# Kernel optimization log

Measured on AMD Instinct MI355X. Metric: run time of the kernel, lower is better.

## Reference

```python
import jax, jax.numpy as jnp
import numpy as np

NUM_SYM = 50000
NUM_HERB = 50000
N_NODES = NUM_SYM + NUM_HERB
DIM = 128
N_EDGES = 3200000
N_LAYERS = 2


def setup_inputs() -> dict:
    key = jax.random.key(0)
    k1, k2, k3, k4, k5 = jax.random.split(key, 5)
    sym_emb = jax.random.normal(k1, (NUM_SYM, DIM), dtype=jnp.float32)
    herb_emb = jax.random.normal(k2, (NUM_HERB, DIM), dtype=jnp.float32)
    adj_rows = jax.random.randint(k3, (N_EDGES,), 0, N_NODES, dtype=jnp.int32)
    adj_cols = jax.random.randint(k4, (N_EDGES,), 0, N_NODES, dtype=jnp.int32)
    # normalized-Laplacian values are positive; uniform stands in for D^-1/2 A D^-1/2 entries
    adj_vals = jax.random.uniform(k5, (N_EDGES,), dtype=jnp.float32)
    return {"sym_emb": sym_emb, "herb_emb": herb_emb,
            "adj_rows": adj_rows, "adj_cols": adj_cols, "adj_vals": adj_vals}


def _spmm(rows, cols, vals, x):
    # sparse [N,N] @ dense [N,D]: gather source rows, scale, scatter-add to dest rows
    msgs = vals[:, None] * x[cols]              # [E, D]
    return jax.ops.segment_sum(msgs, rows, num_segments=N_NODES)


def reference(sym_emb, herb_emb, adj_rows, adj_cols, adj_vals):
    ego = jnp.concatenate([sym_emb, herb_emb], axis=0)   # [N, D]
    acc = ego
    e = ego
    for _ in range(N_LAYERS):
        e = _spmm(adj_rows, adj_cols, adj_vals, e)
        acc = acc + e
    all_emb = acc / jnp.float32(N_LAYERS + 1)            # mean over stacked layers
    return all_emb[:NUM_SYM], all_emb[NUM_SYM:]
```

## Files before the change

### kernel.cpp

```cpp
#include <hip/hip_runtime.h>

#define NUM_SYM 50000
#define NUM_HERB 50000
#define N_NODES (NUM_SYM + NUM_HERB)
#define DIM 128
#define NB_BUCKETS ((N_NODES + 255) / 256)
#define CHUNK 8192
#define PAD 16

typedef float floatx4 __attribute__((ext_vector_type(4)));

__device__ __forceinline__ float bf2f(unsigned short u) {
    return __uint_as_float((unsigned)u << 16);
}
__device__ __forceinline__ unsigned short f2bf(float f) {
    unsigned u = __float_as_uint(f);
    unsigned r = (u + 0x7FFFu + ((u >> 16) & 1u)) >> 16;
    return (unsigned short)r;
}

__global__ __launch_bounds__(256) void to_bf16(
    const float* __restrict__ sym, const float* __restrict__ herb,
    ushort* __restrict__ xbf)
{
    int i = blockIdx.x * 256 + threadIdx.x;
    const int n4 = N_NODES * DIM / 4;
    if (i >= n4) return;
    const int sym4 = NUM_SYM * DIM / 4;
    float4 v = (i < sym4) ? reinterpret_cast<const float4*>(sym)[i]
                          : reinterpret_cast<const float4*>(herb)[i - sym4];
    ushort4 o;
    o.x = f2bf(v.x); o.y = f2bf(v.y); o.z = f2bf(v.z); o.w = f2bf(v.w);
    reinterpret_cast<ushort4*>(xbf)[i] = o;
}


__global__ __launch_bounds__(1024) void hist_buckets(
    const int* __restrict__ rows, int E, int* __restrict__ bucket_cnt)
{
    __shared__ int h[NB_BUCKETS];
    for (int i = threadIdx.x; i < NB_BUCKETS; i += 1024) h[i] = 0;
    __syncthreads();
    int start = blockIdx.x * CHUNK;
    int end   = min(start + CHUNK, E);
    for (int e = start + threadIdx.x; e < end; e += 1024)
        atomicAdd(&h[rows[e] >> 8], 1);
    __syncthreads();
    for (int i = threadIdx.x; i < NB_BUCKETS; i += 1024)
        if (h[i]) atomicAdd(&bucket_cnt[i * PAD], h[i]);
}

__global__ __launch_bounds__(512) void scan_buckets(
    const int* __restrict__ cnt, int* __restrict__ off, int* __restrict__ cursor)
{
    __shared__ int s[512];
    int t = threadIdx.x;
    int v = (t < NB_BUCKETS) ? cnt[t * PAD] : 0;
    s[t] = v;
    __syncthreads();
    for (int o = 1; o < 512; o <<= 1) {
        int x = (t >= o) ? s[t - o] : 0;
        __syncthreads();
        s[t] += x;
        __syncthreads();
    }
    if (t < NB_BUCKETS) { off[t] = s[t] - v; cursor[t * PAD] = s[t] - v; }
    if (t == NB_BUCKETS - 1) off[NB_BUCKETS] = s[t];
}

__global__ __launch_bounds__(1024) void scatter_buckets(
    const int* __restrict__ rows, const int* __restrict__ cols,
    const float* __restrict__ vals, int E,
    int* __restrict__ cursor, int2* __restrict__ bucketed)
{
    __shared__ int lh[NB_BUCKETS];
    __shared__ int lbase[NB_BUCKETS];
    for (int i = threadIdx.x; i < NB_BUCKETS; i += 1024) lh[i] = 0;
    __syncthreads();
    int start = blockIdx.x * CHUNK;
    int end   = min(start + CHUNK, E);
    for (int e = start + threadIdx.x; e < end; e += 1024)
        atomicAdd(&lh[rows[e] >> 8], 1);
    __syncthreads();
    for (int i = threadIdx.x; i < NB_BUCKETS; i += 1024) {
        int c = lh[i];
        lbase[i] = c ? atomicAdd(&cursor[i * PAD], c) : 0;
        lh[i] = 0;
    }
    __syncthreads();
    for (int e = start + threadIdx.x; e < end; e += 1024) {
        int r = rows[e];
        int key = r >> 8;
        int pos = lbase[key] + atomicAdd(&lh[key], 1);
        bucketed[pos] = make_int2(((r & 255) << 17) | cols[e],
                                  __float_as_int(vals[e]));
    }
}

__global__ __launch_bounds__(1024) void bucket_to_csr(
    const int2* __restrict__ bucketed, const int* __restrict__ off,
    int* __restrict__ csr, int* __restrict__ rowptr)
{
    __shared__ int h[256];
    int b = blockIdx.x, t = threadIdx.x;
    int s0 = off[b], s1 = off[b + 1];
    if (t < 256) h[t] = 0;
    __syncthreads();
    for (int j = s0 + t; j < s1; j += 1024)
        atomicAdd(&h[(unsigned)bucketed[j].x >> 17], 1);
    __syncthreads();
    int v = (t < 256) ? h[t] : 0;
    for (int o = 1; o < 256; o <<= 1) {
        int x = (t < 256 && t >= o) ? h[t - o] : 0;
        __syncthreads();
        if (t < 256) h[t] += x;
        __syncthreads();
    }
    if (t < 256) {
        int r = b * 256 + t;
        if (r < N_NODES) rowptr[r] = s0 + (h[t] - v);
    }
    __syncthreads();
    if (t < 256) h[t] -= v;
    __syncthreads();
    for (int j = s0 + t; j < s1; j += 1024) {
        int2 rec = bucketed[j];
        int key = (unsigned)rec.x >> 17;
        int pos = s0 + atomicAdd(&h[key], 1);
        unsigned vb = (unsigned)f2bf(__int_as_float(rec.y));
        csr[pos] = (int)((vb << 17) | ((unsigned)rec.x & 0x1FFFFu));
    }
}

__device__ __forceinline__ float unpack_val(int p) {
    return __uint_as_float(((unsigned)p >> 17) << 16);
}

template <bool FUSE_MEAN>
__global__ __launch_bounds__(256) void spmm_csr_bf16(
    const int* __restrict__ csr, const int* __restrict__ rowptr, int E,
    const ushort* __restrict__ xbf,
    const float* __restrict__ sym, const float* __restrict__ herb,
    const ushort* __restrict__ e1bf,
    void* __restrict__ outp)
{
    int wave = blockIdx.x * 4 + (threadIdx.x >> 6);
    int half = (threadIdx.x >> 5) & 1;
    int lane = threadIdx.x & 31;
    int r = wave * 2 + half;
    if (r >= N_NODES) return;

    int j   = rowptr[r];
    int end = (r + 1 < N_NODES) ? rowptr[r + 1] : E;

    float4 acc = make_float4(0.f, 0.f, 0.f, 0.f);
    for (; j + 7 < end; j += 8) {
        int p0 = __builtin_nontemporal_load(csr + j);
        int p1 = __builtin_nontemporal_load(csr + j + 1);
        int p2 = __builtin_nontemporal_load(csr + j + 2);
        int p3 = __builtin_nontemporal_load(csr + j + 3);
        int p4 = __builtin_nontemporal_load(csr + j + 4);
        int p5 = __builtin_nontemporal_load(csr + j + 5);
        int p6 = __builtin_nontemporal_load(csr + j + 6);
        int p7 = __builtin_nontemporal_load(csr + j + 7);
        ushort4 m0 = reinterpret_cast<const ushort4*>(xbf + (size_t)(p0 & 0x1FFFF) * DIM)[lane];
        ushort4 m1 = reinterpret_cast<const ushort4*>(xbf + (size_t)(p1 & 0x1FFFF) * DIM)[lane];
        ushort4 m2 = reinterpret_cast<const ushort4*>(xbf + (size_t)(p2 & 0x1FFFF) * DIM)[lane];
        ushort4 m3 = reinterpret_cast<const ushort4*>(xbf + (size_t)(p3 & 0x1FFFF) * DIM)[lane];
        ushort4 m4 = reinterpret_cast<const ushort4*>(xbf + (size_t)(p4 & 0x1FFFF) * DIM)[lane];
        ushort4 m5 = reinterpret_cast<const ushort4*>(xbf + (size_t)(p5 & 0x1FFFF) * DIM)[lane];
        ushort4 m6 = reinterpret_cast<const ushort4*>(xbf + (size_t)(p6 & 0x1FFFF) * DIM)[lane];
        ushort4 m7 = reinterpret_cast<const ushort4*>(xbf + (size_t)(p7 & 0x1FFFF) * DIM)[lane];
        float v0 = unpack_val(p0), v1 = unpack_val(p1);
        float v2 = unpack_val(p2), v3 = unpack_val(p3);
        float v4 = unpack_val(p4), v5 = unpack_val(p5);
        float v6 = unpack_val(p6), v7 = unpack_val(p7);
        acc.x += v0 * bf2f(m0.x) + v1 * bf2f(m1.x) + v2 * bf2f(m2.x) + v3 * bf2f(m3.x)
               + v4 * bf2f(m4.x) + v5 * bf2f(m5.x) + v6 * bf2f(m6.x) + v7 * bf2f(m7.x);
        acc.y += v0 * bf2f(m0.y) + v1 * bf2f(m1.y) + v2 * bf2f(m2.y) + v3 * bf2f(m3.y)
               + v4 * bf2f(m4.y) + v5 * bf2f(m5.y) + v6 * bf2f(m6.y) + v7 * bf2f(m7.y);
        acc.z += v0 * bf2f(m0.z) + v1 * bf2f(m1.z) + v2 * bf2f(m2.z) + v3 * bf2f(m3.z)
               + v4 * bf2f(m4.z) + v5 * bf2f(m5.z) + v6 * bf2f(m6.z) + v7 * bf2f(m7.z);
        acc.w += v0 * bf2f(m0.w) + v1 * bf2f(m1.w) + v2 * bf2f(m2.w) + v3 * bf2f(m3.w)
               + v4 * bf2f(m4.w) + v5 * bf2f(m5.w) + v6 * bf2f(m6.w) + v7 * bf2f(m7.w);
    }
    for (; j + 3 < end; j += 4) {
        int p0 = __builtin_nontemporal_load(csr + j);
        int p1 = __builtin_nontemporal_load(csr + j + 1);
        int p2 = __builtin_nontemporal_load(csr + j + 2);
        int p3 = __builtin_nontemporal_load(csr + j + 3);
        ushort4 m0 = reinterpret_cast<const ushort4*>(xbf + (size_t)(p0 & 0x1FFFF) * DIM)[lane];
        ushort4 m1 = reinterpret_cast<const ushort4*>(xbf + (size_t)(p1 & 0x1FFFF) * DIM)[lane];
        ushort4 m2 = reinterpret_cast<const ushort4*>(xbf + (size_t)(p2 & 0x1FFFF) * DIM)[lane];
        ushort4 m3 = reinterpret_cast<const ushort4*>(xbf + (size_t)(p3 & 0x1FFFF) * DIM)[lane];
        float v0 = unpack_val(p0), v1 = unpack_val(p1);
        float v2 = unpack_val(p2), v3 = unpack_val(p3);
        acc.x += v0 * bf2f(m0.x) + v1 * bf2f(m1.x) + v2 * bf2f(m2.x) + v3 * bf2f(m3.x);
        acc.y += v0 * bf2f(m0.y) + v1 * bf2f(m1.y) + v2 * bf2f(m2.y) + v3 * bf2f(m3.y);
        acc.z += v0 * bf2f(m0.z) + v1 * bf2f(m1.z) + v2 * bf2f(m2.z) + v3 * bf2f(m3.z);
        acc.w += v0 * bf2f(m0.w) + v1 * bf2f(m1.w) + v2 * bf2f(m2.w) + v3 * bf2f(m3.w);
    }
    for (; j < end; ++j) {
        int p0 = __builtin_nontemporal_load(csr + j);
        float v0 = unpack_val(p0);
        ushort4 m0 = reinterpret_cast<const ushort4*>(xbf + (size_t)(p0 & 0x1FFFF) * DIM)[lane];
        acc.x += v0 * bf2f(m0.x);
        acc.y += v0 * bf2f(m0.y);
        acc.z += v0 * bf2f(m0.z);
        acc.w += v0 * bf2f(m0.w);
    }

    if (FUSE_MEAN) {
        const float4* egorow = (r < NUM_SYM)
            ? reinterpret_cast<const float4*>(sym  + (size_t)r * DIM)
            : reinterpret_cast<const float4*>(herb + (size_t)(r - NUM_SYM) * DIM);
        float4 g = egorow[lane];
        ushort4 a = reinterpret_cast<const ushort4*>(e1bf + (size_t)r * DIM)[lane];
        const float s = 1.0f / 3.0f;
        floatx4 o;
        o.x = (g.x + bf2f(a.x) + acc.x) * s;
        o.y = (g.y + bf2f(a.y) + acc.y) * s;
        o.z = (g.z + bf2f(a.z) + acc.z) * s;
        o.w = (g.w + bf2f(a.w) + acc.w) * s;
        __builtin_nontemporal_store(o,
            reinterpret_cast<floatx4*>((float*)outp + (size_t)r * DIM) + lane);
    } else {
        ushort4 o;
        o.x = f2bf(acc.x); o.y = f2bf(acc.y); o.z = f2bf(acc.z); o.w = f2bf(acc.w);
        reinterpret_cast<ushort4*>((ushort*)outp + (size_t)r * DIM)[lane] = o;
    }
}

__global__ __launch_bounds__(256) void spmm_scatter(
    const int* __restrict__ rows, const int* __restrict__ cols,
    const float* __restrict__ vals, int n_edges,
    const float* __restrict__ xa, const float* __restrict__ xb,
    float* __restrict__ out)
{
    int gid = blockIdx.x * 256 + threadIdx.x;
    int edge = gid >> 5;
    if (edge >= n_edges) return;
    int sub = gid & 31;
    int c = cols[edge];
    int r = rows[edge];
    float v = vals[edge];
    const float* xrow = (c < NUM_SYM) ? (xa + (size_t)c * DIM)
                                      : (xb + (size_t)(c - NUM_SYM) * DIM);
    float4 m = reinterpret_cast<const float4*>(xrow)[sub];
    float* o = out + (size_t)r * DIM + (size_t)sub * 4;
    unsafeAtomicAdd(o + 0, v * m.x);
    unsafeAtomicAdd(o + 1, v * m.y);
    unsafeAtomicAdd(o + 2, v * m.z);
    unsafeAtomicAdd(o + 3, v * m.w);
}

__global__ __launch_bounds__(256) void finalize_mean(
    const float* __restrict__ sym, const float* __restrict__ herb,
    const float* __restrict__ e1, float* __restrict__ out)
{
    int i = blockIdx.x * 256 + threadIdx.x;
    const int n4 = N_NODES * DIM / 4;
    if (i >= n4) return;
    const int sym4 = NUM_SYM * DIM / 4;
    float4 e = (i < sym4) ? reinterpret_cast<const float4*>(sym)[i]
                          : reinterpret_cast<const float4*>(herb)[i - sym4];
    float4 a = reinterpret_cast<const float4*>(e1)[i];
    float4 b = reinterpret_cast<float4*>(out)[i];
    const float s = 1.0f / 3.0f;
    float4 r;
    r.x = (e.x + a.x + b.x) * s;
    r.y = (e.y + a.y + b.y) * s;
    r.z = (e.z + a.z + b.z) * s;
    r.w = (e.w + a.w + b.w) * s;
    reinterpret_cast<float4*>(out)[i] = r;
}

extern "C" void kernel_launch(void* const* d_in, const int* in_sizes, int n_in,
                              void* d_out, int out_size, void* d_ws, size_t ws_size,
                              hipStream_t stream) {
    const float* sym  = (const float*)d_in[0];
    const float* herb = (const float*)d_in[1];
    const int*   rows = (const int*)d_in[2];
    const int*   cols = (const int*)d_in[3];
    const float* vals = (const float*)d_in[4];
    const int E = in_sizes[2];
    float* out = (float*)d_out;

    char* ws = (char*)d_ws;
    auto align256 = [](size_t x) { return (x + 255) & ~(size_t)255; };
    const size_t xbf_bytes   = (size_t)N_NODES * DIM * sizeof(ushort);
    const size_t csr_off     = align256(xbf_bytes);
    const size_t buck_off    = align256(csr_off + (size_t)E * 4);
    const size_t buck_bytes  = (size_t)E * 8 > xbf_bytes ? (size_t)E * 8 : xbf_bytes;
    const size_t rowptr_off  = align256(buck_off + buck_bytes);
    const size_t bcnt_off    = align256(rowptr_off + (size_t)N_NODES * 4);
    const size_t boff_off    = align256(bcnt_off + (size_t)NB_BUCKETS * PAD * 4);
    const size_t bcur_off    = align256(boff_off + (size_t)(NB_BUCKETS + 1) * 4);
    const size_t required    = bcur_off + (size_t)NB_BUCKETS * PAD * 4;

    if (ws_size < required || E >= (1 << 22)) {
        float* e1 = (float*)ws;
        const size_t e1_bytes = (size_t)N_NODES * DIM * sizeof(float);
        hipMemsetAsync(e1, 0, e1_bytes, stream);
        hipMemsetAsync(out, 0, e1_bytes, stream);
        const int spmm_blocks = (E * 32 + 255) / 256;
        spmm_scatter<<<spmm_blocks, 256, 0, stream>>>(rows, cols, vals, E, sym, herb, e1);
        spmm_scatter<<<spmm_blocks, 256, 0, stream>>>(rows, cols, vals, E,
                                                      e1, e1 + (size_t)NUM_SYM * DIM, out);
        const int n4 = N_NODES * DIM / 4;
        finalize_mean<<<(n4 + 255) / 256, 256, 0, stream>>>(sym, herb, e1, out);
        return;
    }

    ushort* xbf      = (ushort*)ws;
    int*    csr      = (int*)(ws + csr_off);
    int2*   bucketed = (int2*)(ws + buck_off);
    ushort* e1bf     = (ushort*)(ws + buck_off);
    int*    rowptr   = (int*)(ws + rowptr_off);
    int*    bcnt     = (int*)(ws + bcnt_off);
    int*    boff     = (int*)(ws + boff_off);
    int*    bcur     = (int*)(ws + bcur_off);

    hipMemsetAsync(bcnt, 0, (size_t)NB_BUCKETS * PAD * 4, stream);
    const int EB = (E + CHUNK - 1) / CHUNK;
    hist_buckets<<<EB, 1024, 0, stream>>>(rows, E, bcnt);
    scan_buckets<<<1, 512, 0, stream>>>(bcnt, boff, bcur);
    scatter_buckets<<<EB, 1024, 0, stream>>>(rows, cols, vals, E, bcur, bucketed);
    bucket_to_csr<<<NB_BUCKETS, 1024, 0, stream>>>(bucketed, boff, csr, rowptr);

    const int n4 = N_NODES * DIM / 4;
    to_bf16<<<(n4 + 255) / 256, 256, 0, stream>>>(sym, herb, xbf);

    const int blocks = (N_NODES / 2 + 3) / 4;
    spmm_csr_bf16<false><<<blocks, 256, 0, stream>>>(csr, rowptr, E, xbf,
                                                     nullptr, nullptr, nullptr, e1bf);
    spmm_csr_bf16<true><<<blocks, 256, 0, stream>>>(csr, rowptr, E, e1bf,
                                                    sym, herb, e1bf, out);
}
```

Before: 462.3 us.

## Sort CSR columns within rows into sub-bins and drop nontemporal index loads

The bucket-to-CSR pass now histograms on (row, column>>13), giving 4096 bins, so each row's edges come out roughly grouped by source-column range. This should make the SpMM gathers more cache-local. The prefix scan is widened to 1024 threads with 4 bins each. The bucketing chunk size is halved, and the SpMM index loads switch from nontemporal to normal cached loads. In exchange the CSR build uses more shared memory and a longer scan.

```diff
diff --git a/kernel.cpp b/kernel.cpp
--- a/kernel.cpp
+++ b/kernel.cpp
@@ -5,7 +5,7 @@
 #define N_NODES (NUM_SYM + NUM_HERB)
 #define DIM 128
 #define NB_BUCKETS ((N_NODES + 255) / 256)
-#define CHUNK 8192
+#define CHUNK 4096
 #define PAD 16
 
 typedef float floatx4 __attribute__((ext_vector_type(4)));
@@ -101,34 +101,48 @@
     const int2* __restrict__ bucketed, const int* __restrict__ off,
     int* __restrict__ csr, int* __restrict__ rowptr)
 {
-    __shared__ int h[256];
+    __shared__ int h[4096];
+    __shared__ int s[1024];
     int b = blockIdx.x, t = threadIdx.x;
     int s0 = off[b], s1 = off[b + 1];
-    if (t < 256) h[t] = 0;
-    __syncthreads();
-    for (int j = s0 + t; j < s1; j += 1024)
-        atomicAdd(&h[(unsigned)bucketed[j].x >> 17], 1);
-    __syncthreads();
-    int v = (t < 256) ? h[t] : 0;
-    for (int o = 1; o < 256; o <<= 1) {
-        int x = (t < 256 && t >= o) ? h[t - o] : 0;
+    #pragma unroll
+    for (int i = 0; i < 4; ++i) h[t + i * 1024] = 0;
+    __syncthreads();
+    for (int j = s0 + t; j < s1; j += 1024) {
+        unsigned x = (unsigned)bucketed[j].x;
+        int bin = (int)(((x >> 17) << 4) | ((x & 0x1FFFFu) >> 13));
+        atomicAdd(&h[bin], 1);
+    }
+    __syncthreads();
+    int base = t * 4;
+    int a0 = h[base], a1 = h[base + 1], a2 = h[base + 2], a3 = h[base + 3];
+    int sum = a0 + a1 + a2 + a3;
+    s[t] = sum;
+    __syncthreads();
+    for (int o = 1; o < 1024; o <<= 1) {
+        int x = (t >= o) ? s[t - o] : 0;
         __syncthreads();
-        if (t < 256) h[t] += x;
+        s[t] += x;
         __syncthreads();
     }
+    int excl = s[t] - sum;
+    h[base]     = excl;
+    h[base + 1] = excl + a0;
+    h[base + 2] = excl + a0 + a1;
+    h[base + 3] = excl + a0 + a1 + a2;
+    __syncthreads();
     if (t < 256) {
         int r = b * 256 + t;
-        if (r < N_NODES) rowptr[r] = s0 + (h[t] - v);
-    }
-    __syncthreads();
-    if (t < 256) h[t] -= v;
+        if (r < N_NODES) rowptr[r] = s0 + h[t * 16];
+    }
     __syncthreads();
     for (int j = s0 + t; j < s1; j += 1024) {
         int2 rec = bucketed[j];
-        int key = (unsigned)rec.x >> 17;
-        int pos = s0 + atomicAdd(&h[key], 1);
+        unsigned x = (unsigned)rec.x;
+        int bin = (int)(((x >> 17) << 4) | ((x & 0x1FFFFu) >> 13));
+        int pos = s0 + atomicAdd(&h[bin], 1);
         unsigned vb = (unsigned)f2bf(__int_as_float(rec.y));
-        csr[pos] = (int)((vb << 17) | ((unsigned)rec.x & 0x1FFFFu));
+        csr[pos] = (int)((vb << 17) | (x & 0x1FFFFu));
     }
 }
 
@@ -155,14 +169,8 @@
 
     float4 acc = make_float4(0.f, 0.f, 0.f, 0.f);
     for (; j + 7 < end; j += 8) {
-        int p0 = __builtin_nontemporal_load(csr + j);
-        int p1 = __builtin_nontemporal_load(csr + j + 1);
-        int p2 = __builtin_nontemporal_load(csr + j + 2);
-        int p3 = __builtin_nontemporal_load(csr + j + 3);
-        int p4 = __builtin_nontemporal_load(csr + j + 4);
-        int p5 = __builtin_nontemporal_load(csr + j + 5);
-        int p6 = __builtin_nontemporal_load(csr + j + 6);
-        int p7 = __builtin_nontemporal_load(csr + j + 7);
+        int p0 = csr[j], p1 = csr[j + 1], p2 = csr[j + 2], p3 = csr[j + 3];
+        int p4 = csr[j + 4], p5 = csr[j + 5], p6 = csr[j + 6], p7 = csr[j + 7];
         ushort4 m0 = reinterpret_cast<const ushort4*>(xbf + (size_t)(p0 & 0x1FFFF) * DIM)[lane];
         ushort4 m1 = reinterpret_cast<const ushort4*>(xbf + (size_t)(p1 & 0x1FFFF) * DIM)[lane];
         ushort4 m2 = reinterpret_cast<const ushort4*>(xbf + (size_t)(p2 & 0x1FFFF) * DIM)[lane];
@@ -185,10 +193,7 @@
                + v4 * bf2f(m4.w) + v5 * bf2f(m5.w) + v6 * bf2f(m6.w) + v7 * bf2f(m7.w);
     }
     for (; j + 3 < end; j += 4) {
-        int p0 = __builtin_nontemporal_load(csr + j);
-        int p1 = __builtin_nontemporal_load(csr + j + 1);
-        int p2 = __builtin_nontemporal_load(csr + j + 2);
-        int p3 = __builtin_nontemporal_load(csr + j + 3);
+        int p0 = csr[j], p1 = csr[j + 1], p2 = csr[j + 2], p3 = csr[j + 3];
         ushort4 m0 = reinterpret_cast<const ushort4*>(xbf + (size_t)(p0 & 0x1FFFF) * DIM)[lane];
         ushort4 m1 = reinterpret_cast<const ushort4*>(xbf + (size_t)(p1 & 0x1FFFF) * DIM)[lane];
         ushort4 m2 = reinterpret_cast<const ushort4*>(xbf + (size_t)(p2 & 0x1FFFF) * DIM)[lane];
@@ -201,7 +206,7 @@
         acc.w += v0 * bf2f(m0.w) + v1 * bf2f(m1.w) + v2 * bf2f(m2.w) + v3 * bf2f(m3.w);
     }
     for (; j < end; ++j) {
-        int p0 = __builtin_nontemporal_load(csr + j);
+        int p0 = csr[j];
         float v0 = unpack_val(p0);
         ushort4 m0 = reinterpret_cast<const ushort4*>(xbf + (size_t)(p0 & 0x1FFFF) * DIM)[lane];
         acc.x += v0 * bf2f(m0.x);
```

After: 452.3 us. -2.2%, faster.

## Split bucket cursors into 8 sub-cursors per bucket and halve chunk size

Applied to the files above, without the earlier changes.

Global bucket counters and cursors are split into 8 groups selected by block index, with the scan producing per-group offsets within each bucket, so global atomics from scatter blocks spread over more addresses. CHUNK is halved, doubling the number of histogram and scatter blocks for more parallelism. The nontemporal loads of CSR entries in the SpMM are replaced with plain loads. The cost is more global atomics in total and a larger counter memset and scan.

```diff
diff --git a/kernel.cpp b/kernel.cpp
--- a/kernel.cpp
+++ b/kernel.cpp
@@ -5,7 +5,8 @@
 #define N_NODES (NUM_SYM + NUM_HERB)
 #define DIM 128
 #define NB_BUCKETS ((N_NODES + 255) / 256)
-#define CHUNK 8192
+#define CHUNK 4096
+#define NG 8
 #define PAD 16
 
 typedef float floatx4 __attribute__((ext_vector_type(4)));
@@ -36,47 +37,63 @@
 
 
 __global__ __launch_bounds__(1024) void hist_buckets(
-    const int* __restrict__ rows, int E, int* __restrict__ bucket_cnt)
+    const int* __restrict__ rows, int E, int* __restrict__ bcnt8)
 {
     __shared__ int h[NB_BUCKETS];
     for (int i = threadIdx.x; i < NB_BUCKETS; i += 1024) h[i] = 0;
     __syncthreads();
+    int g = blockIdx.x & (NG - 1);
     int start = blockIdx.x * CHUNK;
     int end   = min(start + CHUNK, E);
     for (int e = start + threadIdx.x; e < end; e += 1024)
         atomicAdd(&h[rows[e] >> 8], 1);
     __syncthreads();
     for (int i = threadIdx.x; i < NB_BUCKETS; i += 1024)
-        if (h[i]) atomicAdd(&bucket_cnt[i * PAD], h[i]);
-}
-
-__global__ __launch_bounds__(512) void scan_buckets(
-    const int* __restrict__ cnt, int* __restrict__ off, int* __restrict__ cursor)
-{
-    __shared__ int s[512];
-    int t = threadIdx.x;
-    int v = (t < NB_BUCKETS) ? cnt[t * PAD] : 0;
-    s[t] = v;
-    __syncthreads();
-    for (int o = 1; o < 512; o <<= 1) {
-        int x = (t >= o) ? s[t - o] : 0;
+        if (h[i]) atomicAdd(&bcnt8[(i * NG + g) * PAD], h[i]);
+}
+
+__global__ __launch_bounds__(1024) void scan_buckets(
+    const int* __restrict__ bcnt8, int* __restrict__ boff, int* __restrict__ bcur8)
+{
+    __shared__ int s[1024];
+    int c = threadIdx.x;
+    int pre[NG];
+    int tot = 0;
+    if (c < NB_BUCKETS) {
+        #pragma unroll
+        for (int g = 0; g < NG; ++g) {
+            pre[g] = tot;
+            tot += bcnt8[(c * NG + g) * PAD];
+        }
+    }
+    s[c] = tot;
+    __syncthreads();
+    for (int o = 1; o < 1024; o <<= 1) {
+        int x = (c >= o) ? s[c - o] : 0;
         __syncthreads();
-        s[t] += x;
+        s[c] += x;
         __syncthreads();
     }
-    if (t < NB_BUCKETS) { off[t] = s[t] - v; cursor[t * PAD] = s[t] - v; }
-    if (t == NB_BUCKETS - 1) off[NB_BUCKETS] = s[t];
+    int excl = s[c] - tot;
+    if (c < NB_BUCKETS) {
+        boff[c] = excl;
+        #pragma unroll
+        for (int g = 0; g < NG; ++g)
+            bcur8[(c * NG + g) * PAD] = excl + pre[g];
+    }
+    if (c == NB_BUCKETS - 1) boff[NB_BUCKETS] = s[c];
 }
 
 __global__ __launch_bounds__(1024) void scatter_buckets(
     const int* __restrict__ rows, const int* __restrict__ cols,
     const float* __restrict__ vals, int E,
-    int* __restrict__ cursor, int2* __restrict__ bucketed)
+    int* __restrict__ bcur8, int2* __restrict__ bucketed)
 {
     __shared__ int lh[NB_BUCKETS];
     __shared__ int lbase[NB_BUCKETS];
     for (int i = threadIdx.x; i < NB_BUCKETS; i += 1024) lh[i] = 0;
     __syncthreads();
+    int g = blockIdx.x & (NG - 1);
     int start = blockIdx.x * CHUNK;
     int end   = min(start + CHUNK, E);
     for (int e = start + threadIdx.x; e < end; e += 1024)
@@ -84,7 +101,7 @@
     __syncthreads();
     for (int i = threadIdx.x; i < NB_BUCKETS; i += 1024) {
         int c = lh[i];
-        lbase[i] = c ? atomicAdd(&cursor[i * PAD], c) : 0;
+        lbase[i] = c ? atomicAdd(&bcur8[(i * NG + g) * PAD], c) : 0;
         lh[i] = 0;
     }
     __syncthreads();
@@ -155,14 +172,8 @@
 
     float4 acc = make_float4(0.f, 0.f, 0.f, 0.f);
     for (; j + 7 < end; j += 8) {
-        int p0 = __builtin_nontemporal_load(csr + j);
-        int p1 = __builtin_nontemporal_load(csr + j + 1);
-        int p2 = __builtin_nontemporal_load(csr + j + 2);
-        int p3 = __builtin_nontemporal_load(csr + j + 3);
-        int p4 = __builtin_nontemporal_load(csr + j + 4);
-        int p5 = __builtin_nontemporal_load(csr + j + 5);
-        int p6 = __builtin_nontemporal_load(csr + j + 6);
-        int p7 = __builtin_nontemporal_load(csr + j + 7);
+        int p0 = csr[j], p1 = csr[j + 1], p2 = csr[j + 2], p3 = csr[j + 3];
+        int p4 = csr[j + 4], p5 = csr[j + 5], p6 = csr[j + 6], p7 = csr[j + 7];
         ushort4 m0 = reinterpret_cast<const ushort4*>(xbf + (size_t)(p0 & 0x1FFFF) * DIM)[lane];
         ushort4 m1 = reinterpret_cast<const ushort4*>(xbf + (size_t)(p1 & 0x1FFFF) * DIM)[lane];
         ushort4 m2 = reinterpret_cast<const ushort4*>(xbf + (size_t)(p2 & 0x1FFFF) * DIM)[lane];
@@ -185,10 +196,7 @@
                + v4 * bf2f(m4.w) + v5 * bf2f(m5.w) + v6 * bf2f(m6.w) + v7 * bf2f(m7.w);
     }
     for (; j + 3 < end; j += 4) {
-        int p0 = __builtin_nontemporal_load(csr + j);
-        int p1 = __builtin_nontemporal_load(csr + j + 1);
-        int p2 = __builtin_nontemporal_load(csr + j + 2);
-        int p3 = __builtin_nontemporal_load(csr + j + 3);
+        int p0 = csr[j], p1 = csr[j + 1], p2 = csr[j + 2], p3 = csr[j + 3];
         ushort4 m0 = reinterpret_cast<const ushort4*>(xbf + (size_t)(p0 & 0x1FFFF) * DIM)[lane];
         ushort4 m1 = reinterpret_cast<const ushort4*>(xbf + (size_t)(p1 & 0x1FFFF) * DIM)[lane];
         ushort4 m2 = reinterpret_cast<const ushort4*>(xbf + (size_t)(p2 & 0x1FFFF) * DIM)[lane];
@@ -201,7 +209,7 @@
         acc.w += v0 * bf2f(m0.w) + v1 * bf2f(m1.w) + v2 * bf2f(m2.w) + v3 * bf2f(m3.w);
     }
     for (; j < end; ++j) {
-        int p0 = __builtin_nontemporal_load(csr + j);
+        int p0 = csr[j];
         float v0 = unpack_val(p0);
         ushort4 m0 = reinterpret_cast<const ushort4*>(xbf + (size_t)(p0 & 0x1FFFF) * DIM)[lane];
         acc.x += v0 * bf2f(m0.x);
@@ -294,9 +302,9 @@
     const size_t buck_bytes  = (size_t)E * 8 > xbf_bytes ? (size_t)E * 8 : xbf_bytes;
     const size_t rowptr_off  = align256(buck_off + buck_bytes);
     const size_t bcnt_off    = align256(rowptr_off + (size_t)N_NODES * 4);
-    const size_t boff_off    = align256(bcnt_off + (size_t)NB_BUCKETS * PAD * 4);
+    const size_t boff_off    = align256(bcnt_off + (size_t)NB_BUCKETS * NG * PAD * 4);
     const size_t bcur_off    = align256(boff_off + (size_t)(NB_BUCKETS + 1) * 4);
-    const size_t required    = bcur_off + (size_t)NB_BUCKETS * PAD * 4;
+    const size_t required    = bcur_off + (size_t)NB_BUCKETS * NG * PAD * 4;
 
     if (ws_size < required || E >= (1 << 22)) {
         float* e1 = (float*)ws;
@@ -317,15 +325,15 @@
     int2*   bucketed = (int2*)(ws + buck_off);
     ushort* e1bf     = (ushort*)(ws + buck_off);
     int*    rowptr   = (int*)(ws + rowptr_off);
-    int*    bcnt     = (int*)(ws + bcnt_off);
+    int*    bcnt8    = (int*)(ws + bcnt_off);
     int*    boff     = (int*)(ws + boff_off);
-    int*    bcur     = (int*)(ws + bcur_off);
-
-    hipMemsetAsync(bcnt, 0, (size_t)NB_BUCKETS * PAD * 4, stream);
+    int*    bcur8    = (int*)(ws + bcur_off);
+
+    hipMemsetAsync(bcnt8, 0, (size_t)NB_BUCKETS * NG * PAD * 4, stream);
     const int EB = (E + CHUNK - 1) / CHUNK;
-    hist_buckets<<<EB, 1024, 0, stream>>>(rows, E, bcnt);
-    scan_buckets<<<1, 512, 0, stream>>>(bcnt, boff, bcur);
-    scatter_buckets<<<EB, 1024, 0, stream>>>(rows, cols, vals, E, bcur, bucketed);
+    hist_buckets<<<EB, 1024, 0, stream>>>(rows, E, bcnt8);
+    scan_buckets<<<1, 1024, 0, stream>>>(bcnt8, boff, bcur8);
+    scatter_buckets<<<EB, 1024, 0, stream>>>(rows, cols, vals, E, bcur8, bucketed);
     bucket_to_csr<<<NB_BUCKETS, 1024, 0, stream>>>(bucketed, boff, csr, rowptr);
 
     const int n4 = N_NODES * DIM / 4;
```

Result: faster. 443.0 us (-4.2%).
